# Kernel tuning notes

Hardware: AMD Instinct MI355X
Metric: run time of the kernel (lower is better)

## Reference

```python
import jax, jax.numpy as jnp
import numpy as np

B, F, T, D, U = 4096, 256, 128, 6, 16  # batch, features, n_trees, depth, units
NB = 2 ** D  # number of leaf bins


def sparsemax(z):
    # sparsemax over the last axis (matches tfa.activations.sparsemax default axis=-1)
    d = z.shape[-1]
    z_sorted = -jnp.sort(-z, axis=-1)
    k = jnp.arange(1, d + 1, dtype=z.dtype)
    z_cumsum = jnp.cumsum(z_sorted, axis=-1)
    support = (1 + k * z_sorted) > z_cumsum
    k_z = jnp.sum(support, axis=-1, keepdims=True)
    tau = (jnp.take_along_axis(z_cumsum, k_z - 1, axis=-1) - 1.0) / k_z.astype(z.dtype)
    return jnp.maximum(z - tau, 0.0)


def bin_codes_1hot(depth):
    # (depth, 2^depth, 2) one-hot binary codes, as in build()
    idx = np.arange(2 ** depth)
    off = 2 ** np.arange(depth)
    codes = (idx[None, :] // off[:, None]) % 2  # (depth, 2^depth)
    return jnp.asarray(np.stack([codes, 1 - codes], axis=-1), dtype=jnp.float32)


def setup_inputs() -> dict:
    key = jax.random.key(0)
    k1, k2, k3, k4 = jax.random.split(key, 4)
    x = jax.random.normal(k1, (B, F), dtype=jnp.float32)
    feature_selection_logits = jax.random.normal(k2, (F, T, D), dtype=jnp.float32)
    feature_thresholds = 0.1 * jax.random.normal(k3, (T, D), dtype=jnp.float32)
    log_temperatures = jnp.zeros((T, D), dtype=jnp.float32)
    response = jax.random.normal(k4, (T, U, NB), dtype=jnp.float32)
    return {
        "x": x,
        "feature_selection_logits": feature_selection_logits,
        "feature_thresholds": feature_thresholds,
        "log_temperatures": log_temperatures,
        "response": response,
    }


def reference(x, feature_selection_logits, feature_thresholds, log_temperatures, response):
    depth = feature_thresholds.shape[-1]
    codes = bin_codes_1hot(depth)  # (D, 2^D, 2)
    # feature selection
    selectors = sparsemax(feature_selection_logits)          # (F, T, D)
    feature_values = jnp.einsum('bi,ind->bnd', x, selectors)  # (B, T, D)
    # sigmoid-style binarization via sparsemoid
    tl = (feature_values - feature_thresholds) * jnp.exp(-log_temperatures)
    tl = jnp.stack([-tl, tl], axis=-1)                        # (B, T, D, 2)
    bins = jnp.clip(0.5 * tl + 0.5, 0.0, 1.0)                 # sparsemoid
    # one-hot bin matching and product over depth
    bin_matches = jnp.einsum('btds,dcs->btdc', bins, codes)   # (B, T, D, 2^D)
    response_weights = jnp.prod(bin_matches, axis=-2)         # (B, T, 2^D)
    out = jnp.einsum('bnd,ncd->bnc', response_weights, response)  # (B, T, U)
    return jnp.sum(out, axis=1)                               # (B, U)
```

## Files before the change

### kernel.cpp

```cpp
#include <hip/hip_runtime.h>
#include <math.h>

#define B_  4096
#define F_  256
#define T_  128
#define D_  6
#define U_  16
#define NB_ 64
#define N_  (T_ * D_)

typedef __attribute__((ext_vector_type(8))) short bf16x8;
typedef __attribute__((ext_vector_type(4))) float f32x4;

__device__ __forceinline__ short f2b(float f) {
    union { float f; unsigned u; } v; v.f = f;
    unsigned r = (v.u + 0x7FFFu + ((v.u >> 16) & 1u)) >> 16;
    return (short)r;
}
__device__ __forceinline__ float clamp01(float x) {
    return fminf(fmaxf(x, 0.f), 1.f);
}

__global__ __launch_bounds__(256) void prep(const float* __restrict__ fsl,
                                            const float* __restrict__ th,
                                            const float* __restrict__ lt,
                                            const float* __restrict__ resp,
                                            unsigned short* __restrict__ sel_t,
                                            unsigned short* __restrict__ resp_b,
                                            float2* __restrict__ tsc) {
    int bid = blockIdx.x, tid = threadIdx.x;
    if (bid < 128) {
        int r = bid * 256 + tid;
        const float* zp = fsl + (size_t)r * 6;
        float v0 = zp[0], v1 = zp[1], v2 = zp[2], v3 = zp[3], v4 = zp[4], v5 = zp[5];
        float s0 = v0, s1 = v1, s2 = v2, s3 = v3, s4 = v4, s5 = v5;
#define CE(a, b) { float hi_ = fmaxf(a, b), lo_ = fminf(a, b); a = hi_; b = lo_; }
        CE(s0, s1) CE(s2, s3) CE(s4, s5)
        CE(s1, s2) CE(s3, s4)
        CE(s0, s1) CE(s2, s3) CE(s4, s5)
        CE(s1, s2) CE(s3, s4)
        CE(s0, s1) CE(s2, s3) CE(s4, s5)
        CE(s1, s2) CE(s3, s4)
#undef CE
        float cum = 0.f, num = 0.f, kz = 1.f;
        cum += s0; num = cum; kz = 1.f;
        cum += s1; if (1.f + 2.f * s1 > cum) { num = cum; kz = 2.f; }
        cum += s2; if (1.f + 3.f * s2 > cum) { num = cum; kz = 3.f; }
        cum += s3; if (1.f + 4.f * s3 > cum) { num = cum; kz = 4.f; }
        cum += s4; if (1.f + 5.f * s4 > cum) { num = cum; kz = 5.f; }
        cum += s5; if (1.f + 6.f * s5 > cum) { num = cum; kz = 6.f; }
        float tau = (num - 1.f) / kz;
        int f = r >> 7, t = r & 127;
        unsigned short* o = sel_t + f;
        o[(t * 6 + 0) * 256] = (unsigned short)f2b(fmaxf(v0 - tau, 0.f));
        o[(t * 6 + 1) * 256] = (unsigned short)f2b(fmaxf(v1 - tau, 0.f));
        o[(t * 6 + 2) * 256] = (unsigned short)f2b(fmaxf(v2 - tau, 0.f));
        o[(t * 6 + 3) * 256] = (unsigned short)f2b(fmaxf(v3 - tau, 0.f));
        o[(t * 6 + 4) * 256] = (unsigned short)f2b(fmaxf(v4 - tau, 0.f));
        o[(t * 6 + 5) * 256] = (unsigned short)f2b(fmaxf(v5 - tau, 0.f));
    } else if (bid < 256) {
        int i = (bid - 128) * 256 + tid;
        float4 v = *(const float4*)(resp + (size_t)4 * i);
        ushort4 o;
        o.x = (unsigned short)f2b(v.x); o.y = (unsigned short)f2b(v.y);
        o.z = (unsigned short)f2b(v.z); o.w = (unsigned short)f2b(v.w);
        *(ushort4*)(resp_b + (size_t)4 * i) = o;
    } else {
        for (int i = tid; i < N_; i += 256) {
            float s = expf(-lt[i]);
            tsc[i] = make_float2(s, -th[i] * s);
        }
    }
}

#define FVP 772

__global__ __launch_bounds__(512) void fused_gemm_leafsum(
        const float* __restrict__ x,
        const unsigned short* __restrict__ sel_t,
        const unsigned short* __restrict__ resp_b,
        const float2* __restrict__ tsc,
        float* __restrict__ out) {
    __shared__ float fvs[16][FVP];
    __shared__ float red[8][16][17];
    int tid = threadIdx.x;
    int lane = tid & 63;
    int wave = tid >> 6;
    int b0 = blockIdx.x * 16;
    int lm = lane & 15;
    int kq = lane >> 4;

    {
        f32x4 acc[6] = {};
#pragma unroll
        for (int ks = 0; ks < 8; ks++) {
            int k0 = ks * 32 + kq * 8;
            const float* ap = x + (size_t)(b0 + lm) * F_ + k0;
            float4 f0 = *(const float4*)ap;
            float4 f1 = *(const float4*)(ap + 4);
            bf16x8 a;
            a[0] = f2b(f0.x); a[1] = f2b(f0.y); a[2] = f2b(f0.z); a[3] = f2b(f0.w);
            a[4] = f2b(f1.x); a[5] = f2b(f1.y); a[6] = f2b(f1.z); a[7] = f2b(f1.w);
#pragma unroll
            for (int i = 0; i < 6; i++) {
                int n = (wave * 6 + i) * 16 + lm;
                bf16x8 b = *(const bf16x8*)(sel_t + (size_t)n * F_ + k0);
                acc[i] = __builtin_amdgcn_mfma_f32_16x16x32_bf16(a, b, acc[i], 0, 0, 0);
            }
        }
#pragma unroll
        for (int i = 0; i < 6; i++) {
            int n0 = (wave * 6 + i) * 16;
#pragma unroll
            for (int r = 0; r < 4; r++)
                fvs[kq * 4 + r][n0 + lm] = acc[i][r];
        }
    }
    __syncthreads();

    f32x4 acc = {};
    int q0 = kq & 1, q1 = kq >> 1;
    for (int t = wave; t < T_; t += 8) {
        float bp[6], bn[6];
#pragma unroll
        for (int d = 0; d < 6; d++) {
            float2 so = tsc[t * 6 + d];
            float tl = fmaf(fvs[lm][t * 6 + d], so.x, so.y);
            bp[d] = clamp01(fmaf(tl, 0.5f, 0.5f));
            bn[d] = clamp01(fmaf(tl, -0.5f, 0.5f));
        }
        float p01[4] = { bp[0] * bp[1], bn[0] * bp[1], bp[0] * bn[1], bn[0] * bn[1] };
        float p3[8];
#pragma unroll
        for (int j = 0; j < 8; j++) p3[j] = p01[j & 3] * ((j & 4) ? bn[2] : bp[2]);
        float t34 = (q0 ? bn[3] : bp[3]) * (q1 ? bn[4] : bp[4]);
        float w0 = t34 * bp[5], w1 = t34 * bn[5];
        bf16x8 a0, a1;
#pragma unroll
        for (int j = 0; j < 8; j++) {
            a0[j] = f2b(p3[j] * w0);
            a1[j] = f2b(p3[j] * w1);
        }
        const unsigned short* rbp = resp_b + (size_t)t * (U_ * NB_) + lm * NB_ + kq * 8;
        bf16x8 br0 = *(const bf16x8*)rbp;
        bf16x8 br1 = *(const bf16x8*)(rbp + 32);
        acc = __builtin_amdgcn_mfma_f32_16x16x32_bf16(a0, br0, acc, 0, 0, 0);
        acc = __builtin_amdgcn_mfma_f32_16x16x32_bf16(a1, br1, acc, 0, 0, 0);
    }
#pragma unroll
    for (int r = 0; r < 4; r++) red[wave][kq * 4 + r][lm] = acc[r];
    __syncthreads();
    if (tid < 256) {
        int row = tid >> 4, col = tid & 15;
        float s = 0.f;
#pragma unroll
        for (int w = 0; w < 8; w++) s += red[w][row][col];
        out[(size_t)(b0 + row) * U_ + col] = s;
    }
}

extern "C" void kernel_launch(void* const* d_in, const int* in_sizes, int n_in,
                              void* d_out, int out_size, void* d_ws, size_t ws_size,
                              hipStream_t stream) {
    const float* x    = (const float*)d_in[0];
    const float* fsl  = (const float*)d_in[1];
    const float* th   = (const float*)d_in[2];
    const float* lt   = (const float*)d_in[3];
    const float* resp = (const float*)d_in[4];
    float* out = (float*)d_out;

    char* w = (char*)d_ws;
    unsigned short* sel_t  = (unsigned short*)w;
    unsigned short* resp_b = (unsigned short*)(w + 393216);
    float2*         tsc    = (float2*)(w + 655360);

    prep<<<dim3(257), dim3(256), 0, stream>>>(fsl, th, lt, resp, sel_t, resp_b, tsc);
    fused_gemm_leafsum<<<dim3(B_ / 16), dim3(512), 0, stream>>>(x, sel_t, resp_b, tsc, out);
}
```

Baseline: 89.40 us.

## Use packed bf16 conversion, pad fvs per tree, pre-apply threshold scaling

Replaces the manual bf16 rounding with packed float2-to-bfloat162 conversions so two values are converted per instruction (likely mapping to the native packed convert on gfx950). The feature-value shared buffer is relaid out with 8 floats per tree, so the leaf stage can read the six depth values with vector LDS loads. The threshold and temperature affine is now applied in a separate cooperative pass instead of per wave per tree. This adds an extra barrier and a larger shared-memory footprint in exchange for less ALU and fewer global tsc loads in the inner loop.

After: 87.31 us. 2.3% less time.

```diff
diff --git a/kernel.cpp b/kernel.cpp
--- a/kernel.cpp
+++ b/kernel.cpp
@@ -1,4 +1,5 @@
 #include <hip/hip_runtime.h>
+#include <hip/hip_bf16.h>
 #include <math.h>
 
 #define B_  4096
@@ -16,6 +17,11 @@
     union { float f; unsigned u; } v; v.f = f;
     unsigned r = (v.u + 0x7FFFu + ((v.u >> 16) & 1u)) >> 16;
     return (short)r;
+}
+__device__ __forceinline__ unsigned pk2(float lo, float hi) {
+    union { __hip_bfloat162 h; unsigned u; } c;
+    c.h = __float22bfloat162_rn(make_float2(lo, hi));
+    return c.u;
 }
 __device__ __forceinline__ float clamp01(float x) {
     return fminf(fmaxf(x, 0.f), 1.f);
@@ -61,10 +67,10 @@
     } else if (bid < 256) {
         int i = (bid - 128) * 256 + tid;
         float4 v = *(const float4*)(resp + (size_t)4 * i);
-        ushort4 o;
-        o.x = (unsigned short)f2b(v.x); o.y = (unsigned short)f2b(v.y);
-        o.z = (unsigned short)f2b(v.z); o.w = (unsigned short)f2b(v.w);
-        *(ushort4*)(resp_b + (size_t)4 * i) = o;
+        uint2 o;
+        o.x = pk2(v.x, v.y);
+        o.y = pk2(v.z, v.w);
+        *(uint2*)(resp_b + (size_t)4 * i) = o;
     } else {
         for (int i = tid; i < N_; i += 256) {
             float s = expf(-lt[i]);
@@ -73,7 +79,7 @@
     }
 }
 
-#define FVP 772
+#define FVP 1028
 
 __global__ __launch_bounds__(512) void fused_gemm_leafsum(
         const float* __restrict__ x,
@@ -98,22 +104,37 @@
             const float* ap = x + (size_t)(b0 + lm) * F_ + k0;
             float4 f0 = *(const float4*)ap;
             float4 f1 = *(const float4*)(ap + 4);
-            bf16x8 a;
-            a[0] = f2b(f0.x); a[1] = f2b(f0.y); a[2] = f2b(f0.z); a[3] = f2b(f0.w);
-            a[4] = f2b(f1.x); a[5] = f2b(f1.y); a[6] = f2b(f1.z); a[7] = f2b(f1.w);
+            union { bf16x8 v; unsigned u[4]; } a;
+            a.u[0] = pk2(f0.x, f0.y); a.u[1] = pk2(f0.z, f0.w);
+            a.u[2] = pk2(f1.x, f1.y); a.u[3] = pk2(f1.z, f1.w);
 #pragma unroll
             for (int i = 0; i < 6; i++) {
                 int n = (wave * 6 + i) * 16 + lm;
                 bf16x8 b = *(const bf16x8*)(sel_t + (size_t)n * F_ + k0);
-                acc[i] = __builtin_amdgcn_mfma_f32_16x16x32_bf16(a, b, acc[i], 0, 0, 0);
+                acc[i] = __builtin_amdgcn_mfma_f32_16x16x32_bf16(a.v, b, acc[i], 0, 0, 0);
             }
         }
 #pragma unroll
         for (int i = 0; i < 6; i++) {
-            int n0 = (wave * 6 + i) * 16;
+            int n = (wave * 6 + i) * 16 + lm;
+            int t = n / 6, d = n - t * 6;
+            int col = t * 8 + d;
 #pragma unroll
             for (int r = 0; r < 4; r++)
-                fvs[kq * 4 + r][n0 + lm] = acc[i][r];
+                fvs[kq * 4 + r][col] = acc[i][r];
+        }
+    }
+    __syncthreads();
+
+    {
+        int b = tid & 15;
+        int chunk = tid >> 4;
+#pragma unroll
+        for (int j = 0; j < 24; j++) {
+            int n = chunk * 24 + j;
+            float2 so = tsc[n];
+            int col = (chunk * 4 + j / 6) * 8 + (j % 6);
+            fvs[b][col] = fmaf(fvs[b][col], so.x, so.y);
         }
     }
     __syncthreads();
@@ -121,13 +142,14 @@
     f32x4 acc = {};
     int q0 = kq & 1, q1 = kq >> 1;
     for (int t = wave; t < T_; t += 8) {
+        float4 tl03 = *(const float4*)&fvs[lm][t * 8];
+        float2 tl45 = *(const float2*)&fvs[lm][t * 8 + 4];
+        float tl[6] = { tl03.x, tl03.y, tl03.z, tl03.w, tl45.x, tl45.y };
         float bp[6], bn[6];
 #pragma unroll
         for (int d = 0; d < 6; d++) {
-            float2 so = tsc[t * 6 + d];
-            float tl = fmaf(fvs[lm][t * 6 + d], so.x, so.y);
-            bp[d] = clamp01(fmaf(tl, 0.5f, 0.5f));
-            bn[d] = clamp01(fmaf(tl, -0.5f, 0.5f));
+            bp[d] = clamp01(fmaf(tl[d],  0.5f, 0.5f));
+            bn[d] = clamp01(fmaf(tl[d], -0.5f, 0.5f));
         }
         float p01[4] = { bp[0] * bp[1], bn[0] * bp[1], bp[0] * bn[1], bn[0] * bn[1] };
         float p3[8];
@@ -135,17 +157,17 @@
         for (int j = 0; j < 8; j++) p3[j] = p01[j & 3] * ((j & 4) ? bn[2] : bp[2]);
         float t34 = (q0 ? bn[3] : bp[3]) * (q1 ? bn[4] : bp[4]);
         float w0 = t34 * bp[5], w1 = t34 * bn[5];
-        bf16x8 a0, a1;
-#pragma unroll
-        for (int j = 0; j < 8; j++) {
-            a0[j] = f2b(p3[j] * w0);
-            a1[j] = f2b(p3[j] * w1);
+        union { bf16x8 v; unsigned u[4]; } a0, a1;
+#pragma unroll
+        for (int j = 0; j < 4; j++) {
+            a0.u[j] = pk2(p3[2 * j] * w0, p3[2 * j + 1] * w0);
+            a1.u[j] = pk2(p3[2 * j] * w1, p3[2 * j + 1] * w1);
         }
         const unsigned short* rbp = resp_b + (size_t)t * (U_ * NB_) + lm * NB_ + kq * 8;
         bf16x8 br0 = *(const bf16x8*)rbp;
         bf16x8 br1 = *(const bf16x8*)(rbp + 32);
-        acc = __builtin_amdgcn_mfma_f32_16x16x32_bf16(a0, br0, acc, 0, 0, 0);
-        acc = __builtin_amdgcn_mfma_f32_16x16x32_bf16(a1, br1, acc, 0, 0, 0);
+        acc = __builtin_amdgcn_mfma_f32_16x16x32_bf16(a0.v, br0, acc, 0, 0, 0);
+        acc = __builtin_amdgcn_mfma_f32_16x16x32_bf16(a1.v, br1, acc, 0, 0, 0);
     }
 #pragma unroll
     for (int r = 0; r < 4; r++) red[wave][kq * 4 + r][lm] = acc[r];
```
